# Performance work log

Measured on AMD Instinct MI355X. Metric: run time of the kernel, lower is better.

The kernel has to match this reference:

```python
import jax, jax.numpy as jnp
import numpy as np

B, S = 16384, 2048
EPS = 1e-8


def _autocorr(x, lag):
    # Pearson correlation between x[:, :-lag] and x[:, lag:] (ddof cancels).
    a = x[:, :-lag]
    b = x[:, lag:]
    am = a.mean(axis=1, keepdims=True)
    bm = b.mean(axis=1, keepdims=True)
    cov = ((a - am) * (b - bm)).mean(axis=1)
    return cov / (a.std(axis=1) * b.std(axis=1))


def _stat_features(x):
    S_len = x.shape[1]
    mean = x.mean(axis=1)
    xc = x - mean[:, None]
    m2 = (xc ** 2).mean(axis=1)
    m3 = (xc ** 3).mean(axis=1)
    m4 = (xc ** 4).mean(axis=1)
    std = jnp.sqrt(m2)
    min_v = x.min(axis=1)
    max_v = x.max(axis=1)
    q = jnp.percentile(x, jnp.array([25.0, 50.0, 75.0]), axis=1)  # [3, B]
    p25, median, p75 = q[0], q[1], q[2]
    diff = jnp.diff(x, axis=1)
    std_diff = diff.std(axis=1)
    trend = std_diff / (std + EPS)
    ac1 = _autocorr(x, 1)
    ac7 = _autocorr(x, 7)
    ac24 = _autocorr(x, 24)
    cv = std / (jnp.abs(mean) + EPS)
    iqr = p75 - p25
    seasonal = x[:, ::24].var(axis=1) / (m2 + EPS)
    skew = m3 / (m2 ** 1.5)          # scipy.stats.skew, bias=True
    kurt = m4 / (m2 ** 2) - 3.0      # scipy.stats.kurtosis, Fisher, bias=True
    length = jnp.full_like(mean, float(S_len))
    sum_abs_diff = jnp.abs(diff).sum(axis=1)
    mean_abs_diff = jnp.abs(diff).mean(axis=1)
    feats = jnp.stack([mean, std, min_v, max_v, median, trend, ac1, ac7, ac24,
                       cv, iqr, seasonal, skew, kurt, length,
                       sum_abs_diff, mean_abs_diff, std_diff, p25, p75], axis=1)
    return jnp.where(jnp.isfinite(feats), feats, 0.0)


def setup_inputs() -> dict:
    key = jax.random.key(0)
    k0, k1, k2, k3, k4 = jax.random.split(key, 5)
    x = jax.random.normal(k0, (B, S), dtype=jnp.float32)
    W1 = jax.random.normal(k1, (64, 20), dtype=jnp.float32) * 0.1
    b1 = jnp.zeros((64,), dtype=jnp.float32)
    W2 = jax.random.normal(k3, (128, 64), dtype=jnp.float32) * 0.1
    b2 = jnp.zeros((128,), dtype=jnp.float32)
    return {"x": x, "W1": W1, "b1": b1, "W2": W2, "b2": b2}


def reference(x, W1, b1, W2, b2):
    feats = _stat_features(x)                      # [B, 20]
    h = jax.nn.relu(feats @ W1.T + b1)             # [B, 64] (dropout inactive at eval)
    return h @ W2.T + b2                           # [B, 128]
```

## Files before the change

### kernel.cpp

```cpp
#include <hip/hip_runtime.h>
#include <cmath>

constexpr int S_LEN = 2048;
constexpr float EPS = 1e-8f;

typedef unsigned uvec32 __attribute__((ext_vector_type(32)));

__device__ __forceinline__ float fin(float v) { return isfinite(v) ? v : 0.0f; }

__device__ __forceinline__ unsigned f2o_bits(unsigned u) {
    return (u & 0x80000000u) ? ~u : (u | 0x80000000u);
}
__device__ __forceinline__ float o2f(unsigned u) {
    return __uint_as_float((u & 0x80000000u) ? (u ^ 0x80000000u) : ~u);
}

template <int Ctrl, int Rmask>
__device__ __forceinline__ int dpp_zero_i(int x) {
    return __builtin_amdgcn_update_dpp(0, x, Ctrl, Rmask, 0xF, true);
}
template <int Ctrl>
__device__ __forceinline__ int dpp_keep_i(int x) {
    return __builtin_amdgcn_update_dpp(x, x, Ctrl, 0xF, 0xF, false);
}

__device__ __forceinline__ int wred_add_i(int v) {
    v += dpp_zero_i<0xB1, 0xF>(v);
    v += dpp_zero_i<0x4E, 0xF>(v);
    v += dpp_zero_i<0x114, 0xF>(v);
    v += dpp_zero_i<0x118, 0xF>(v);
    v += dpp_zero_i<0x142, 0xA>(v);
    v += dpp_zero_i<0x143, 0xC>(v);
    return __builtin_amdgcn_readlane(v, 63);
}
__device__ __forceinline__ float wred_add_f(float v) {
    #define ADDF(CT, RM) v += __uint_as_float((unsigned)dpp_zero_i<CT, RM>((int)__float_as_uint(v)))
    ADDF(0xB1, 0xF); ADDF(0x4E, 0xF); ADDF(0x114, 0xF);
    ADDF(0x118, 0xF); ADDF(0x142, 0xA); ADDF(0x143, 0xC);
    #undef ADDF
    return __uint_as_float((unsigned)__builtin_amdgcn_readlane((int)__float_as_uint(v), 63));
}
__device__ __forceinline__ float wred_min_f(float v) {
    #define MINF(CT) v = fminf(v, __uint_as_float((unsigned)dpp_keep_i<CT>((int)__float_as_uint(v))))
    MINF(0xB1); MINF(0x4E); MINF(0x114); MINF(0x118); MINF(0x142); MINF(0x143);
    #undef MINF
    return __uint_as_float((unsigned)__builtin_amdgcn_readlane((int)__float_as_uint(v), 63));
}
__device__ __forceinline__ float wred_max_f(float v) {
    #define MAXF(CT) v = fmaxf(v, __uint_as_float((unsigned)dpp_keep_i<CT>((int)__float_as_uint(v))))
    MAXF(0xB1); MAXF(0x4E); MAXF(0x114); MAXF(0x118); MAXF(0x142); MAXF(0x143);
    #undef MAXF
    return __uint_as_float((unsigned)__builtin_amdgcn_readlane((int)__float_as_uint(v), 63));
}
__device__ __forceinline__ unsigned wred_umin(unsigned v) {
    #define MINU(CT) { unsigned t = (unsigned)dpp_keep_i<CT>((int)v); v = v < t ? v : t; }
    MINU(0xB1) MINU(0x4E) MINU(0x114) MINU(0x118) MINU(0x142) MINU(0x143)
    #undef MINU
    return (unsigned)__builtin_amdgcn_readlane((int)v, 63);
}
__device__ __forceinline__ float readlane_f(float x, int l) {
    return __uint_as_float((unsigned)__builtin_amdgcn_readlane((int)__float_as_uint(x), l));
}

__device__ __forceinline__ void transpose32(uvec32& A) {
    #pragma unroll
    for (int j = 16; j; j >>= 1) {
        unsigned m = (j == 16) ? 0x0000FFFFu : (j == 8) ? 0x00FF00FFu
                   : (j == 4) ? 0x0F0F0F0Fu : (j == 2) ? 0x33333333u : 0x55555555u;
        #pragma unroll
        for (int k = 0; k < 32; k++) {
            if (!(k & j)) {
                unsigned t = (A[k] ^ (A[k | j] >> j)) & m;
                A[k] = A[k] ^ t;
                A[k | j] = A[k | j] ^ (t << j);
            }
        }
    }
}

#define VF(e) __uint_as_float(a[e])

__global__ __launch_bounds__(256)
__attribute__((amdgpu_waves_per_eu(4, 4)))
void stat_feat_kernel(
    const float* __restrict__ x,
    const float* __restrict__ W1, const float* __restrict__ b1,
    const float* __restrict__ W2, const float* __restrict__ b2,
    float* __restrict__ out, int nrows)
{
    __shared__ float w2s[128 * 65];
    __shared__ float w1s[64 * 21];
    __shared__ float featss[4 * 20];
    __shared__ float hs[4 * 64];

    const int tid  = threadIdx.x;
    const int lane = tid & 63;
    const int w    = tid >> 6;
    const int row  = min(blockIdx.x * 4 + w, nrows - 1);

    for (int n = tid; n < 64 * 20; n += 256) w1s[(n / 20) * 21 + (n % 20)] = W1[n];
    #pragma unroll 8
    for (int it = 0; it < 32; it++) {
        int n = tid + 256 * it;
        w2s[(n >> 6) * 65 + (n & 63)] = W2[n];
    }

    uvec32 a;
    const float* xr = x + (size_t)row * S_LEN + lane * 32;
    #pragma unroll
    for (int q = 0; q < 8; q++) {
        float4 t = reinterpret_cast<const float4*>(xr)[q];
        a[4 * q + 0] = __float_as_uint(t.x); a[4 * q + 1] = __float_as_uint(t.y);
        a[4 * q + 2] = __float_as_uint(t.z); a[4 * q + 3] = __float_as_uint(t.w);
    }

    float s1 = 0.f, s2 = 0.f, sd2 = 0.f, sad = 0.f;
    float p1 = 0.f, p7 = 0.f, p24 = 0.f, se1 = 0.f, se2 = 0.f;
    float mn = VF(0), mx = VF(0);
    #pragma unroll
    for (int e = 0; e < 32; e++) {
        float val = VF(e);
        s1 += val; s2 = fmaf(val, val, s2);
        mn = fminf(mn, val); mx = fmaxf(mx, val);
    }
    #pragma unroll
    for (int e = 0; e < 31; e++) {
        float d = VF(e + 1) - VF(e);
        sd2 = fmaf(d, d, sd2); sad += fabsf(d);
        p1 = fmaf(VF(e), VF(e + 1), p1);
    }
    #pragma unroll
    for (int e = 0; e < 25; e++) p7 = fmaf(VF(e), VF(e + 7), p7);
    #pragma unroll
    for (int e = 0; e < 8; e++)  p24 = fmaf(VF(e), VF(e + 24), p24);

    const bool notlast = (lane < 63);
    #pragma unroll
    for (int j = 0; j < 24; j++) {
        float nb = __shfl_down(VF(j), 1, 64);
        float g = notlast ? nb : 0.f;
        p24 = fmaf(VF(8 + j), g, p24);
        if (j < 7) p7 = fmaf(VF(25 + j), g, p7);
        if (j == 0 && notlast) {
            float d = nb - VF(31);
            sd2 = fmaf(d, d, sd2); sad += fabsf(d);
            p1 = fmaf(VF(31), nb, p1);
        }
    }
    {
        int r3 = lane % 3;
        float sv = (r3 == 0) ? VF(0) : ((r3 == 1) ? VF(16) : VF(8));
        se1 += sv; se2 = fmaf(sv, sv, se2);
        if (r3 == 0) { se1 += VF(24); se2 = fmaf(VF(24), VF(24), se2); }
    }

    float aa = 0, bb = 0, h7v = 0, hq7v = 0;
    #pragma unroll
    for (int e = 0; e < 24; e++) {
        aa += VF(e); bb = fmaf(VF(e), VF(e), bb);
        if (e == 6) { h7v = aa; hq7v = bb; }
    }
    float cc = 0, dd = 0, t7v = 0, tq7v = 0;
    #pragma unroll
    for (int e = 31; e >= 8; e--) {
        cc += VF(e); dd = fmaf(VF(e), VF(e), dd);
        if (e == 25) { t7v = cc; tq7v = dd; }
    }
    const float h1  = readlane_f(VF(0), 0),   t1  = readlane_f(VF(31), 63);
    const float h7  = readlane_f(h7v, 0),     hq7 = readlane_f(hq7v, 0);
    const float h24 = readlane_f(aa, 0),      hq24 = readlane_f(bb, 0);
    const float t7  = readlane_f(t7v, 63),    tq7 = readlane_f(tq7v, 63);
    const float t24 = readlane_f(cc, 63),     tq24 = readlane_f(dd, 63);
    const float hq1 = h1 * h1, tq1 = t1 * t1;

    float S1  = wred_add_f(s1);
    float mean = S1 * (1.0f / S_LEN);
    float S2  = wred_add_f(s2);
    float SD2 = wred_add_f(sd2);
    float SAD = wred_add_f(sad);
    float P1  = wred_add_f(p1);
    float P7  = wred_add_f(p7);
    float P24 = wred_add_f(p24);
    float SE1 = wred_add_f(se1);
    float SE2 = wred_add_f(se2);
    float MN  = wred_min_f(mn);
    float MX  = wred_max_f(mx);

    float c2 = 0.f, c3 = 0.f, c4 = 0.f;
    #pragma unroll
    for (int e = 0; e < 32; e++) {
        float xc = VF(e) - mean;
        float q = xc * xc;
        c2 += q; c3 = fmaf(q, xc, c3); c4 = fmaf(q, q, c4);
    }
    float C2 = wred_add_f(c2), C3 = wred_add_f(c3), C4 = wred_add_f(c4);

    const float Sf = (float)S_LEN;
    const float nd = Sf - 1.0f;
    {
        float m2v = C2 / Sf, m3v = C3 / Sf, m4v = C4 / Sf;
        float stdv = sqrtf(m2v);
        float dmean = (t1 - h1) / nd;
        float dvar = SD2 / nd - dmean * dmean;
        float std_diff = sqrtf(fmaxf(dvar, 0.f));
        float trend = std_diff / (stdv + EPS);

        float ac[3];
        const float Ls[3] = {1.f, 7.f, 24.f};
        const float Ps[3] = {P1, P7, P24};
        const float hd[3] = {h1, h7, h24},   hqv[3] = {hq1, hq7, hq24};
        const float tl[3] = {t1, t7, t24},   tqv[3] = {tq1, tq7, tq24};
        #pragma unroll
        for (int q = 0; q < 3; q++) {
            float n = Sf - Ls[q];
            float sa = S1 - tl[q], sb = S1 - hd[q];
            float qa = S2 - tqv[q], qb = S2 - hqv[q];
            float am = sa / n, bm = sb / n;
            float cov = Ps[q] / n - am * bm;
            float as_ = sqrtf(fmaxf(qa / n - am * am, 0.f));
            float bs_ = sqrtf(fmaxf(qb / n - bm * bm, 0.f));
            ac[q] = cov / (as_ * bs_);
        }
        float cv = stdv / (fabsf(mean) + EPS);
        float sm = SE1 / 86.f;
        float svar = SE2 / 86.f - sm * sm;
        float seasonal = svar / (m2v + EPS);
        float skew = m3v / (m2v * stdv);
        float kurt = m4v / (m2v * m2v) - 3.f;

        if (lane == 0) {
            float* fp = &featss[w * 20];
            fp[0] = fin(mean);      fp[1] = fin(stdv);
            fp[2] = fin(MN);        fp[3] = fin(MX);
            fp[5] = fin(trend);
            fp[6] = fin(ac[0]);     fp[7] = fin(ac[1]);
            fp[8] = fin(ac[2]);     fp[9] = fin(cv);
            fp[11] = fin(seasonal);
            fp[12] = fin(skew);     fp[13] = fin(kurt);
            fp[14] = Sf;            fp[15] = fin(SAD);
            fp[16] = fin(SAD / nd); fp[17] = fin(std_diff);
        }
    }

    #pragma unroll
    for (int e = 0; e < 32; e++) a[e] = f2o_bits(a[e]);
    transpose32(a);

    unsigned act0 = ~0u, act1 = ~0u, act2 = ~0u;
    int K0 = 511, K1 = 1023, K2 = 1535;
    unsigned uK0 = 0, uK1 = 0, uK2 = 0;
    #pragma unroll
    for (int b = 31; b >= 0; b--) {
        unsigned mb = a[31 - b];
        unsigned z0 = act0 & ~mb, z1 = act1 & ~mb, z2 = act2 & ~mb;
        int C01 = wred_add_i(__popc(z0) | (__popc(z1) << 16));
        int Cc2 = wred_add_i(__popc(z2));
        int c0 = C01 & 0xFFFF;
        int c1 = (int)((unsigned)C01 >> 16);
        if (K0 < c0)  act0 = z0; else { K0 -= c0;  act0 &= mb; uK0 |= (1u << b); }
        if (K1 < c1)  act1 = z1; else { K1 -= c1;  act1 &= mb; uK1 |= (1u << b); }
        if (K2 < Cc2) act2 = z2; else { K2 -= Cc2; act2 &= mb; uK2 |= (1u << b); }
    }
    int e01 = wred_add_i(__popc(act0) | (__popc(act1) << 16));
    int eq0 = e01 & 0xFFFF, eq1 = (int)((unsigned)e01 >> 16);
    int eq2 = wred_add_i(__popc(act2));

    transpose32(a);
    unsigned m0 = ~0u, m1 = ~0u, m2 = ~0u;
    #pragma unroll
    for (int e = 0; e < 32; e++) {
        unsigned ue = a[e];
        if (ue > uK0) m0 = m0 < ue ? m0 : ue;
        if (ue > uK1) m1 = m1 < ue ? m1 : ue;
        if (ue > uK2) m2 = m2 < ue ? m2 : ue;
    }
    m0 = wred_umin(m0); m1 = wred_umin(m1); m2 = wred_umin(m2);
    {
        float v511 = o2f(uK0), v1023 = o2f(uK1), v1535 = o2f(uK2);
        float v512  = (K0 + 1 < eq0) ? v511  : o2f(m0);
        float v1024 = (K1 + 1 < eq1) ? v1023 : o2f(m1);
        float v1536 = (K2 + 1 < eq2) ? v1535 : o2f(m2);
        float p25 = v511 + 0.75f * (v512 - v511);
        float med = 0.5f * (v1023 + v1024);
        float p75 = v1535 + 0.25f * (v1536 - v1535);
        float iqr = p75 - p25;
        if (lane == 0) {
            float* fp = &featss[w * 20];
            fp[4]  = fin(med);
            fp[10] = fin(iqr);
            fp[18] = fin(p25);
            fp[19] = fin(p75);
        }
    }
    __syncthreads();

    {
        float acc = b1[lane];
        #pragma unroll
        for (int j = 0; j < 20; j++)
            acc = fmaf(featss[w * 20 + j], w1s[lane * 21 + j], acc);
        hs[w * 64 + lane] = fmaxf(acc, 0.f);
    }
    __syncthreads();
    {
        int j  = tid & 127;
        int r0 = tid >> 7;
        int r1 = r0 + 2;
        float acc0 = b2[j], acc1 = acc0;
        #pragma unroll
        for (int k = 0; k < 64; k++) {
            float wv2 = w2s[j * 65 + k];
            acc0 = fmaf(hs[r0 * 64 + k], wv2, acc0);
            acc1 = fmaf(hs[r1 * 64 + k], wv2, acc1);
        }
        size_t rb = (size_t)blockIdx.x * 4;
        if ((int)(rb + r0) < nrows) out[(rb + r0) * 128 + j] = acc0;
        if ((int)(rb + r1) < nrows) out[(rb + r1) * 128 + j] = acc1;
    }
}

extern "C" void kernel_launch(void* const* d_in, const int* in_sizes, int n_in,
                              void* d_out, int out_size, void* d_ws, size_t ws_size,
                              hipStream_t stream) {
    const float* x  = (const float*)d_in[0];
    const float* W1 = (const float*)d_in[1];
    const float* b1 = (const float*)d_in[2];
    const float* W2 = (const float*)d_in[3];
    const float* b2 = (const float*)d_in[4];
    float* out = (float*)d_out;
    int nrows = in_sizes[0] / S_LEN;
    int blocks = (nrows + 3) / 4;
    stat_feat_kernel<<<blocks, 256, 0, stream>>>(x, W1, b1, W2, b2, out, nrows);
}
```

Measured before the change: 328.5 us.

## Split fused kernel into stats, percentile and MLP kernels via workspace

The single fused kernel is split into three launches. The first computes moment and autocorrelation features, the second computes percentiles, and the third runs the MLP on features stored in the workspace. This removes the per-block shared-memory staging of W1/W2 and the waves_per_eu restriction, which may lower register and LDS pressure per kernel. In exchange, x is read twice from global memory, there are extra launches, and features make a round trip through memory. The MLP kernel reads weights uncoalesced straight from global memory and uses readlane.

```diff
diff --git a/kernel.cpp b/kernel.cpp
--- a/kernel.cpp
+++ b/kernel.cpp
@@ -80,33 +80,15 @@
 
 #define VF(e) __uint_as_float(a[e])
 
-__global__ __launch_bounds__(256)
-__attribute__((amdgpu_waves_per_eu(4, 4)))
-void stat_feat_kernel(
-    const float* __restrict__ x,
-    const float* __restrict__ W1, const float* __restrict__ b1,
-    const float* __restrict__ W2, const float* __restrict__ b2,
-    float* __restrict__ out, int nrows)
+__global__ __launch_bounds__(256) void stats_kernel(
+    const float* __restrict__ x, float* __restrict__ feats, int nrows)
 {
-    __shared__ float w2s[128 * 65];
-    __shared__ float w1s[64 * 21];
-    __shared__ float featss[4 * 20];
-    __shared__ float hs[4 * 64];
-
-    const int tid  = threadIdx.x;
-    const int lane = tid & 63;
-    const int w    = tid >> 6;
-    const int row  = min(blockIdx.x * 4 + w, nrows - 1);
-
-    for (int n = tid; n < 64 * 20; n += 256) w1s[(n / 20) * 21 + (n % 20)] = W1[n];
-    #pragma unroll 8
-    for (int it = 0; it < 32; it++) {
-        int n = tid + 256 * it;
-        w2s[(n >> 6) * 65 + (n & 63)] = W2[n];
-    }
+    const int gw   = (blockIdx.x * 256 + threadIdx.x) >> 6;
+    const int lane = threadIdx.x & 63;
+    if (gw >= nrows) return;
 
     uvec32 a;
-    const float* xr = x + (size_t)row * S_LEN + lane * 32;
+    const float* xr = x + (size_t)gw * S_LEN + lane * 32;
     #pragma unroll
     for (int q = 0; q < 8; q++) {
         float4 t = reinterpret_cast<const float4*>(xr)[q];
@@ -197,15 +179,15 @@
 
     const float Sf = (float)S_LEN;
     const float nd = Sf - 1.0f;
+    float m2v = C2 / Sf, m3v = C3 / Sf, m4v = C4 / Sf;
+    float stdv = sqrtf(m2v);
+    float dmean = (t1 - h1) / nd;
+    float dvar = SD2 / nd - dmean * dmean;
+    float std_diff = sqrtf(fmaxf(dvar, 0.f));
+    float trend = std_diff / (stdv + EPS);
+
+    float ac[3];
     {
-        float m2v = C2 / Sf, m3v = C3 / Sf, m4v = C4 / Sf;
-        float stdv = sqrtf(m2v);
-        float dmean = (t1 - h1) / nd;
-        float dvar = SD2 / nd - dmean * dmean;
-        float std_diff = sqrtf(fmaxf(dvar, 0.f));
-        float trend = std_diff / (stdv + EPS);
-
-        float ac[3];
         const float Ls[3] = {1.f, 7.f, 24.f};
         const float Ps[3] = {P1, P7, P24};
         const float hd[3] = {h1, h7, h24},   hqv[3] = {hq1, hq7, hq24};
@@ -221,27 +203,43 @@
             float bs_ = sqrtf(fmaxf(qb / n - bm * bm, 0.f));
             ac[q] = cov / (as_ * bs_);
         }
-        float cv = stdv / (fabsf(mean) + EPS);
-        float sm = SE1 / 86.f;
-        float svar = SE2 / 86.f - sm * sm;
-        float seasonal = svar / (m2v + EPS);
-        float skew = m3v / (m2v * stdv);
-        float kurt = m4v / (m2v * m2v) - 3.f;
-
-        if (lane == 0) {
-            float* fp = &featss[w * 20];
-            fp[0] = fin(mean);      fp[1] = fin(stdv);
-            fp[2] = fin(MN);        fp[3] = fin(MX);
-            fp[5] = fin(trend);
-            fp[6] = fin(ac[0]);     fp[7] = fin(ac[1]);
-            fp[8] = fin(ac[2]);     fp[9] = fin(cv);
-            fp[11] = fin(seasonal);
-            fp[12] = fin(skew);     fp[13] = fin(kurt);
-            fp[14] = Sf;            fp[15] = fin(SAD);
-            fp[16] = fin(SAD / nd); fp[17] = fin(std_diff);
-        }
-    }
-
+    }
+    float cv = stdv / (fabsf(mean) + EPS);
+    float sm = SE1 / 86.f;
+    float svar = SE2 / 86.f - sm * sm;
+    float seasonal = svar / (m2v + EPS);
+    float skew = m3v / (m2v * stdv);
+    float kurt = m4v / (m2v * m2v) - 3.f;
+
+    if (lane == 0) {
+        float* fp = feats + (size_t)gw * 20;
+        fp[0] = fin(mean);      fp[1] = fin(stdv);
+        fp[2] = fin(MN);        fp[3] = fin(MX);
+        fp[5] = fin(trend);
+        fp[6] = fin(ac[0]);     fp[7] = fin(ac[1]);
+        fp[8] = fin(ac[2]);     fp[9] = fin(cv);
+        fp[11] = fin(seasonal);
+        fp[12] = fin(skew);     fp[13] = fin(kurt);
+        fp[14] = Sf;            fp[15] = fin(SAD);
+        fp[16] = fin(SAD / nd); fp[17] = fin(std_diff);
+    }
+}
+
+__global__ __launch_bounds__(256) void pct_kernel(
+    const float* __restrict__ x, float* __restrict__ feats, int nrows)
+{
+    const int gw   = (blockIdx.x * 256 + threadIdx.x) >> 6;
+    const int lane = threadIdx.x & 63;
+    if (gw >= nrows) return;
+
+    uvec32 a;
+    const float* xr = x + (size_t)gw * S_LEN + lane * 32;
+    #pragma unroll
+    for (int q = 0; q < 8; q++) {
+        float4 t = reinterpret_cast<const float4*>(xr)[q];
+        a[4 * q + 0] = __float_as_uint(t.x); a[4 * q + 1] = __float_as_uint(t.y);
+        a[4 * q + 2] = __float_as_uint(t.z); a[4 * q + 3] = __float_as_uint(t.w);
+    }
     #pragma unroll
     for (int e = 0; e < 32; e++) a[e] = f2o_bits(a[e]);
     transpose32(a);
@@ -275,48 +273,50 @@
         if (ue > uK2) m2 = m2 < ue ? m2 : ue;
     }
     m0 = wred_umin(m0); m1 = wred_umin(m1); m2 = wred_umin(m2);
-    {
-        float v511 = o2f(uK0), v1023 = o2f(uK1), v1535 = o2f(uK2);
-        float v512  = (K0 + 1 < eq0) ? v511  : o2f(m0);
-        float v1024 = (K1 + 1 < eq1) ? v1023 : o2f(m1);
-        float v1536 = (K2 + 1 < eq2) ? v1535 : o2f(m2);
-        float p25 = v511 + 0.75f * (v512 - v511);
-        float med = 0.5f * (v1023 + v1024);
-        float p75 = v1535 + 0.25f * (v1536 - v1535);
-        float iqr = p75 - p25;
-        if (lane == 0) {
-            float* fp = &featss[w * 20];
-            fp[4]  = fin(med);
-            fp[10] = fin(iqr);
-            fp[18] = fin(p25);
-            fp[19] = fin(p75);
-        }
-    }
-    __syncthreads();
-
-    {
-        float acc = b1[lane];
-        #pragma unroll
-        for (int j = 0; j < 20; j++)
-            acc = fmaf(featss[w * 20 + j], w1s[lane * 21 + j], acc);
-        hs[w * 64 + lane] = fmaxf(acc, 0.f);
-    }
-    __syncthreads();
-    {
-        int j  = tid & 127;
-        int r0 = tid >> 7;
-        int r1 = r0 + 2;
-        float acc0 = b2[j], acc1 = acc0;
-        #pragma unroll
-        for (int k = 0; k < 64; k++) {
-            float wv2 = w2s[j * 65 + k];
-            acc0 = fmaf(hs[r0 * 64 + k], wv2, acc0);
-            acc1 = fmaf(hs[r1 * 64 + k], wv2, acc1);
-        }
-        size_t rb = (size_t)blockIdx.x * 4;
-        if ((int)(rb + r0) < nrows) out[(rb + r0) * 128 + j] = acc0;
-        if ((int)(rb + r1) < nrows) out[(rb + r1) * 128 + j] = acc1;
-    }
+
+    float v511 = o2f(uK0), v1023 = o2f(uK1), v1535 = o2f(uK2);
+    float v512  = (K0 + 1 < eq0) ? v511  : o2f(m0);
+    float v1024 = (K1 + 1 < eq1) ? v1023 : o2f(m1);
+    float v1536 = (K2 + 1 < eq2) ? v1535 : o2f(m2);
+    float p25 = v511 + 0.75f * (v512 - v511);
+    float med = 0.5f * (v1023 + v1024);
+    float p75 = v1535 + 0.25f * (v1536 - v1535);
+    float iqr = p75 - p25;
+
+    if (lane == 0) {
+        float* fp = feats + (size_t)gw * 20;
+        fp[4]  = fin(med);
+        fp[10] = fin(iqr);
+        fp[18] = fin(p25);
+        fp[19] = fin(p75);
+    }
+}
+
+__global__ __launch_bounds__(256) void mlp_kernel(
+    const float* __restrict__ feats,
+    const float* __restrict__ W1, const float* __restrict__ b1,
+    const float* __restrict__ W2, const float* __restrict__ b2,
+    float* __restrict__ out, int nrows)
+{
+    const int gw   = (blockIdx.x * 256 + threadIdx.x) >> 6;
+    const int lane = threadIdx.x & 63;
+    if (gw >= nrows) return;
+
+    const float* fp = feats + (size_t)gw * 20;
+    float h = b1[lane];
+    #pragma unroll
+    for (int j = 0; j < 20; j++) h = fmaf(fp[j], W1[lane * 20 + j], h);
+    h = fmaxf(h, 0.f);
+
+    float o0 = b2[lane], o1 = b2[lane + 64];
+    #pragma unroll
+    for (int k = 0; k < 64; k++) {
+        float hk = readlane_f(h, k);
+        o0 = fmaf(hk, W2[lane * 64 + k], o0);
+        o1 = fmaf(hk, W2[(lane + 64) * 64 + k], o1);
+    }
+    out[(size_t)gw * 128 + lane]      = o0;
+    out[(size_t)gw * 128 + 64 + lane] = o1;
 }
 
 extern "C" void kernel_launch(void* const* d_in, const int* in_sizes, int n_in,
@@ -327,8 +327,11 @@
     const float* b1 = (const float*)d_in[2];
     const float* W2 = (const float*)d_in[3];
     const float* b2 = (const float*)d_in[4];
-    float* out = (float*)d_out;
+    float* out   = (float*)d_out;
+    float* feats = (float*)d_ws;
     int nrows = in_sizes[0] / S_LEN;
     int blocks = (nrows + 3) / 4;
-    stat_feat_kernel<<<blocks, 256, 0, stream>>>(x, W1, b1, W2, b2, out, nrows);
-}
+    stats_kernel<<<blocks, 256, 0, stream>>>(x, feats, nrows);
+    pct_kernel<<<blocks, 256, 0, stream>>>(x, feats, nrows);
+    mlp_kernel<<<blocks, 256, 0, stream>>>(feats, W1, b1, W2, b2, out, nrows);
+}
```

Result: slower. 361.8 us (+10.1%).

## Split fused kernel into stats kernel and persistent MLP kernel

Applied to the files above, without the earlier changes.

Splits the single fused kernel in two. The first kernel computes the 20 features per row without any shared memory and writes them to workspace in a permuted float4 layout. The second is a persistent 512-block MLP kernel that loads W1 (with the column permutation undone) and W2 into LDS once and loops over row groups. The aim is to stop every stats block from reloading roughly 38 KB of weights and to lift the LDS and occupancy limits on the bandwidth-bound stats pass, at the cost of an extra launch and a workspace round trip.

```diff
diff --git a/kernel.cpp b/kernel.cpp
--- a/kernel.cpp
+++ b/kernel.cpp
@@ -23,7 +23,6 @@
 __device__ __forceinline__ int dpp_keep_i(int x) {
     return __builtin_amdgcn_update_dpp(x, x, Ctrl, 0xF, 0xF, false);
 }
-
 __device__ __forceinline__ int wred_add_i(int v) {
     v += dpp_zero_i<0xB1, 0xF>(v);
     v += dpp_zero_i<0x4E, 0xF>(v);
@@ -80,33 +79,16 @@
 
 #define VF(e) __uint_as_float(a[e])
 
-__global__ __launch_bounds__(256)
-__attribute__((amdgpu_waves_per_eu(4, 4)))
-void stat_feat_kernel(
-    const float* __restrict__ x,
-    const float* __restrict__ W1, const float* __restrict__ b1,
-    const float* __restrict__ W2, const float* __restrict__ b2,
-    float* __restrict__ out, int nrows)
+
+__global__ __launch_bounds__(256) void statspct_kernel(
+    const float* __restrict__ x, float* __restrict__ feats, int nrows)
 {
-    __shared__ float w2s[128 * 65];
-    __shared__ float w1s[64 * 21];
-    __shared__ float featss[4 * 20];
-    __shared__ float hs[4 * 64];
-
-    const int tid  = threadIdx.x;
-    const int lane = tid & 63;
-    const int w    = tid >> 6;
-    const int row  = min(blockIdx.x * 4 + w, nrows - 1);
-
-    for (int n = tid; n < 64 * 20; n += 256) w1s[(n / 20) * 21 + (n % 20)] = W1[n];
-    #pragma unroll 8
-    for (int it = 0; it < 32; it++) {
-        int n = tid + 256 * it;
-        w2s[(n >> 6) * 65 + (n & 63)] = W2[n];
-    }
+    const int gw   = (blockIdx.x * 256 + threadIdx.x) >> 6;
+    const int lane = threadIdx.x & 63;
+    if (gw >= nrows) return;
 
     uvec32 a;
-    const float* xr = x + (size_t)row * S_LEN + lane * 32;
+    const float* xr = x + (size_t)gw * S_LEN + lane * 32;
     #pragma unroll
     for (int q = 0; q < 8; q++) {
         float4 t = reinterpret_cast<const float4*>(xr)[q];
@@ -153,7 +135,6 @@
         se1 += sv; se2 = fmaf(sv, sv, se2);
         if (r3 == 0) { se1 += VF(24); se2 = fmaf(VF(24), VF(24), se2); }
     }
-
     float aa = 0, bb = 0, h7v = 0, hq7v = 0;
     #pragma unroll
     for (int e = 0; e < 24; e++) {
@@ -195,16 +176,15 @@
     }
     float C2 = wred_add_f(c2), C3 = wred_add_f(c3), C4 = wred_add_f(c4);
 
-    const float Sf = (float)S_LEN;
-    const float nd = Sf - 1.0f;
     {
+        const float Sf = (float)S_LEN;
+        const float nd = Sf - 1.0f;
         float m2v = C2 / Sf, m3v = C3 / Sf, m4v = C4 / Sf;
         float stdv = sqrtf(m2v);
         float dmean = (t1 - h1) / nd;
         float dvar = SD2 / nd - dmean * dmean;
         float std_diff = sqrtf(fmaxf(dvar, 0.f));
         float trend = std_diff / (stdv + EPS);
-
         float ac[3];
         const float Ls[3] = {1.f, 7.f, 24.f};
         const float Ps[3] = {P1, P7, P24};
@@ -227,18 +207,12 @@
         float seasonal = svar / (m2v + EPS);
         float skew = m3v / (m2v * stdv);
         float kurt = m4v / (m2v * m2v) - 3.f;
-
         if (lane == 0) {
-            float* fp = &featss[w * 20];
-            fp[0] = fin(mean);      fp[1] = fin(stdv);
-            fp[2] = fin(MN);        fp[3] = fin(MX);
-            fp[5] = fin(trend);
-            fp[6] = fin(ac[0]);     fp[7] = fin(ac[1]);
-            fp[8] = fin(ac[2]);     fp[9] = fin(cv);
-            fp[11] = fin(seasonal);
-            fp[12] = fin(skew);     fp[13] = fin(kurt);
-            fp[14] = Sf;            fp[15] = fin(SAD);
-            fp[16] = fin(SAD / nd); fp[17] = fin(std_diff);
+            float4* fp = (float4*)(feats + (size_t)gw * 20);
+            fp[0] = make_float4(fin(mean), fin(stdv), fin(MN), fin(MX));
+            fp[1] = make_float4(fin(trend), fin(ac[0]), fin(ac[1]), fin(ac[2]));
+            fp[2] = make_float4(fin(cv), fin(seasonal), fin(skew), fin(kurt));
+            fp[3] = make_float4(Sf, fin(SAD), fin(SAD / nd), fin(std_diff));
         }
     }
 
@@ -252,7 +226,8 @@
     #pragma unroll
     for (int b = 31; b >= 0; b--) {
         unsigned mb = a[31 - b];
-        unsigned z0 = act0 & ~mb, z1 = act1 & ~mb, z2 = act2 & ~mb;
+        unsigned nmb = ~mb;
+        unsigned z0 = act0 & nmb, z1 = act1 & nmb, z2 = act2 & nmb;
         int C01 = wred_add_i(__popc(z0) | (__popc(z1) << 16));
         int Cc2 = wred_add_i(__popc(z2));
         int c0 = C01 & 0xFFFF;
@@ -275,47 +250,75 @@
         if (ue > uK2) m2 = m2 < ue ? m2 : ue;
     }
     m0 = wred_umin(m0); m1 = wred_umin(m1); m2 = wred_umin(m2);
-    {
-        float v511 = o2f(uK0), v1023 = o2f(uK1), v1535 = o2f(uK2);
-        float v512  = (K0 + 1 < eq0) ? v511  : o2f(m0);
-        float v1024 = (K1 + 1 < eq1) ? v1023 : o2f(m1);
-        float v1536 = (K2 + 1 < eq2) ? v1535 : o2f(m2);
-        float p25 = v511 + 0.75f * (v512 - v511);
-        float med = 0.5f * (v1023 + v1024);
-        float p75 = v1535 + 0.25f * (v1536 - v1535);
-        float iqr = p75 - p25;
-        if (lane == 0) {
-            float* fp = &featss[w * 20];
-            fp[4]  = fin(med);
-            fp[10] = fin(iqr);
-            fp[18] = fin(p25);
-            fp[19] = fin(p75);
-        }
-    }
+
+    float v511 = o2f(uK0), v1023 = o2f(uK1), v1535 = o2f(uK2);
+    float v512  = (K0 + 1 < eq0) ? v511  : o2f(m0);
+    float v1024 = (K1 + 1 < eq1) ? v1023 : o2f(m1);
+    float v1536 = (K2 + 1 < eq2) ? v1535 : o2f(m2);
+    float p25 = v511 + 0.75f * (v512 - v511);
+    float med = 0.5f * (v1023 + v1024);
+    float p75 = v1535 + 0.25f * (v1536 - v1535);
+    float iqr = p75 - p25;
+
+    if (lane == 0) {
+        float4* fp = (float4*)(feats + (size_t)gw * 20);
+        fp[4] = make_float4(fin(med), fin(iqr), fin(p25), fin(p75));
+    }
+}
+
+__global__ __launch_bounds__(256) void mlp_kernel(
+    const float* __restrict__ feats,
+    const float* __restrict__ W1, const float* __restrict__ b1,
+    const float* __restrict__ W2, const float* __restrict__ b2,
+    float* __restrict__ out, int nrows)
+{
+    __shared__ float w2s[128 * 65];
+    __shared__ float w1s[64 * 21];
+    __shared__ float hs[4 * 64];
+
+    static const int perm[20] = {0,1,2,3,5,6,7,8,9,11,12,13,14,15,16,17,4,10,18,19};
+
+    const int tid  = threadIdx.x;
+    const int lane = tid & 63;
+    const int w    = tid >> 6;
+
+    for (int n = tid; n < 64 * 20; n += 256)
+        w1s[(n / 20) * 21 + (n % 20)] = W1[(n / 20) * 20 + perm[n % 20]];
+    #pragma unroll 8
+    for (int it = 0; it < 32; it++) {
+        int n = tid + 256 * it;
+        w2s[(n >> 6) * 65 + (n & 63)] = W2[n];
+    }
+    const float b1v = b1[lane];
+    const int j  = tid & 127;
+    const int r0 = tid >> 7;
+    const float b2v = b2[j];
     __syncthreads();
 
-    {
-        float acc = b1[lane];
-        #pragma unroll
-        for (int j = 0; j < 20; j++)
-            acc = fmaf(featss[w * 20 + j], w1s[lane * 21 + j], acc);
-        hs[w * 64 + lane] = fmaxf(acc, 0.f);
-    }
-    __syncthreads();
-    {
-        int j  = tid & 127;
-        int r0 = tid >> 7;
-        int r1 = r0 + 2;
-        float acc0 = b2[j], acc1 = acc0;
-        #pragma unroll
-        for (int k = 0; k < 64; k++) {
-            float wv2 = w2s[j * 65 + k];
-            acc0 = fmaf(hs[r0 * 64 + k], wv2, acc0);
-            acc1 = fmaf(hs[r1 * 64 + k], wv2, acc1);
-        }
-        size_t rb = (size_t)blockIdx.x * 4;
-        if ((int)(rb + r0) < nrows) out[(rb + r0) * 128 + j] = acc0;
-        if ((int)(rb + r1) < nrows) out[(rb + r1) * 128 + j] = acc1;
+    for (int rg = blockIdx.x * 4; rg < nrows; rg += gridDim.x * 4) {
+        {
+            int row = min(rg + w, nrows - 1);
+            const float* fp = feats + (size_t)row * 20;
+            float acc = b1v;
+            #pragma unroll
+            for (int k = 0; k < 20; k++)
+                acc = fmaf(fp[k], w1s[lane * 21 + k], acc);
+            hs[w * 64 + lane] = fmaxf(acc, 0.f);
+        }
+        __syncthreads();
+        {
+            int r1 = r0 + 2;
+            float acc0 = b2v, acc1 = b2v;
+            #pragma unroll
+            for (int k = 0; k < 64; k++) {
+                float wv2 = w2s[j * 65 + k];
+                acc0 = fmaf(hs[r0 * 64 + k], wv2, acc0);
+                acc1 = fmaf(hs[r1 * 64 + k], wv2, acc1);
+            }
+            if (rg + r0 < nrows) out[(size_t)(rg + r0) * 128 + j] = acc0;
+            if (rg + r1 < nrows) out[(size_t)(rg + r1) * 128 + j] = acc1;
+        }
+        __syncthreads();
     }
 }
 
@@ -327,8 +330,10 @@
     const float* b1 = (const float*)d_in[2];
     const float* W2 = (const float*)d_in[3];
     const float* b2 = (const float*)d_in[4];
-    float* out = (float*)d_out;
+    float* out   = (float*)d_out;
+    float* feats = (float*)d_ws;
     int nrows = in_sizes[0] / S_LEN;
     int blocks = (nrows + 3) / 4;
-    stat_feat_kernel<<<blocks, 256, 0, stream>>>(x, W1, b1, W2, b2, out, nrows);
-}
+    statspct_kernel<<<blocks, 256, 0, stream>>>(x, feats, nrows);
+    mlp_kernel<<<512, 256, 0, stream>>>(feats, W1, b1, W2, b2, out, nrows);
+}
```

Result: faster. 283.8 us (-13.6%).
